# Optimization experiments

Hardware: AMD Instinct MI355X
Metric: run time of the kernel (lower is better)

## Reference

```python
import jax, jax.numpy as jnp
import numpy as np

EPS = 1e-12  # F.normalize default eps


def _l2_normalize(x):
    n = jnp.linalg.norm(x, axis=-1, keepdims=True)
    return x / jnp.maximum(n, EPS)


def setup_inputs() -> dict:
    key = jax.random.key(0)
    k1, k2 = jax.random.split(key)
    B, N, D = 2048, 100000, 256
    query = jax.random.normal(k1, (B, D), dtype=jnp.float32)
    memory_states = jax.random.normal(k2, (N, D), dtype=jnp.float32)
    return {"query": query, "memory_states": memory_states, "k": 8}


def reference(query, memory_states, k):
    # cosine-similarity retrieval: normalize both sides, dense matmul, top-k, gather
    mem_norm = _l2_normalize(memory_states)          # [N, D]
    query_norm = _l2_normalize(query)                # [B, D]
    scores = query_norm @ mem_norm.T                 # [B, N]
    top_k_scores, indices = jax.lax.top_k(scores, k)  # [B, k] each
    retrieved = memory_states[indices]               # [B, k, D] (raw, un-normalized states as in torch)
    return retrieved, top_k_scores
```

## Files before the change

### kernel.cpp

```cpp
#include <hip/hip_runtime.h>
#include <hip/hip_bf16.h>
#include <stdint.h>

#define DIM 256
#define TOPK 8
#define NSTRIPS 64
#define STRIP_TOP 8
#define QT 256
#define NT 32
#define CAND (NSTRIPS * STRIP_TOP)
#define RESCORE 64
#define IDXMASK 0x1FFFFu

typedef __attribute__((ext_vector_type(8))) short short8;
typedef __attribute__((ext_vector_type(4))) float floatx4;
typedef __attribute__((address_space(3))) unsigned int lds_u32;
typedef __attribute__((address_space(1))) const unsigned int gbl_u32;

__device__ __forceinline__ unsigned short f2bf(float f) {
    union { float f; uint32_t u; } v; v.f = f;
    uint32_t u = v.u;
    uint32_t r = u + 0x7fffu + ((u >> 16) & 1u);
    return (unsigned short)(r >> 16);
}

__device__ __forceinline__ uint32_t umaxu(uint32_t a, uint32_t b) { return a > b ? a : b; }

__device__ __forceinline__ void top8_insert(uint32_t* ts, uint32_t key) {
#pragma unroll
    for (int j = 0; j < STRIP_TOP - 1; j++) {
        uint32_t m;
        asm("v_med3_u32 %0, %1, %2, %3" : "=v"(m) : "v"(ts[j]), "v"(ts[j + 1]), "v"(key));
        ts[j] = m;
    }
    ts[STRIP_TOP - 1] = umaxu(ts[STRIP_TOP - 1], key);
}

__global__ void prep_kernel(const float* __restrict__ query,
                            const float* __restrict__ mem,
                            float* __restrict__ rnorm_mem,
                            unsigned short* __restrict__ q_bf16,
                            unsigned short* __restrict__ mem_bf16,
                            int B, int N)
{
    int wave = threadIdx.x >> 6;
    int lane = threadIdx.x & 63;
    int row  = blockIdx.x * 4 + wave;
    int total = N + B;
    if (row >= total) return;
    const float* src = (row < N) ? (mem + (size_t)row * DIM)
                                 : (query + (size_t)(row - N) * DIM);
    float4 v = ((const float4*)src)[lane];
    float ss = v.x * v.x + v.y * v.y + v.z * v.z + v.w * v.w;
#pragma unroll
    for (int m = 32; m >= 1; m >>= 1) ss += __shfl_xor(ss, m, 64);
    float rinv = 1.0f / fmaxf(sqrtf(ss), 1e-12f);
    ushort4 o;
    o.x = f2bf(v.x * rinv); o.y = f2bf(v.y * rinv);
    o.z = f2bf(v.z * rinv); o.w = f2bf(v.w * rinv);
    if (row < N) {
        if (lane == 0) rnorm_mem[row] = rinv;
        if (mem_bf16) ((ushort4*)(mem_bf16 + (size_t)row * DIM))[lane] = o;
    } else {
        ((ushort4*)(q_bf16 + (size_t)(row - N) * DIM))[lane] = o;
    }
}

template<bool PRE>
__global__ __launch_bounds__(512, 4) void score_select_kernel(
    const float* __restrict__ mem,
    const float* __restrict__ rnorm_mem,
    const unsigned short* __restrict__ mem_bf16,
    const unsigned short* __restrict__ q_bf16,
    uint32_t* __restrict__ cand_key,
    int B, int N)
{
    __shared__ unsigned short lds_m[2][NT * DIM];
    __shared__ uint32_t sc[QT * 4 * 9];

    const int t    = threadIdx.x;
    const int wave = t >> 6;
    const int lane = t & 63;
    const int quad = lane >> 4;
    const int l16  = lane & 15;

    const int lin  = (int)(blockIdx.x + gridDim.x * blockIdx.y);
    const int SPX  = NSTRIPS / 8;
    const int strip = (lin & 7) * SPX + ((lin >> 3) % SPX);
    const int qb    = (lin >> 3) / SPX;
    const int qbase = qb * QT;

    const int SS    = (N + NSTRIPS - 1) / NSTRIPS;
    const int n0    = strip * SS;
    const int nend  = (n0 + SS < N) ? (n0 + SS) : N;
    const int limit = nend - n0;
    const int ntiles = (limit + NT - 1) / NT;

    short8 qfrag[2][8];
#pragma unroll
    for (int b = 0; b < 2; b++) {
        int qrow = qbase + wave * 32 + b * 16 + l16;
        const unsigned short* qp = q_bf16 + (size_t)qrow * DIM + quad * 8;
#pragma unroll
        for (int ks = 0; ks < 8; ks++)
            qfrag[b][ks] = *(const short8*)(qp + ks * 32);
    }

    uint32_t ts[2][STRIP_TOP];
#pragma unroll
    for (int b = 0; b < 2; b++)
#pragma unroll
        for (int j = 0; j < STRIP_TOP; j++) ts[b][j] = 0;

    const int l5  = lane >> 5;
    const int s32 = lane & 31;

    auto stage = [&](unsigned short* lbase, int tileIdx) {
        int base = n0 + tileIdx * NT;
        if (PRE) {
#pragma unroll
            for (int is = 0; is < 2; is++) {
                int rl = is * 16 + wave * 2 + l5;
                int n = base + rl; if (n >= nend) n = nend - 1;
                int chunk = s32 ^ (rl & 7);
                const unsigned short* gp = mem_bf16 + (size_t)n * DIM + chunk * 8;
                unsigned short* lp = lbase + (is * 16 + wave * 2) * DIM;
                __builtin_amdgcn_global_load_lds((gbl_u32*)(const void*)gp,
                                                 (lds_u32*)(void*)lp, 16, 0, 0);
            }
        } else {
#pragma unroll
            for (int i = 0; i < 4; i++) {
                int rl = i * 8 + wave;
                int n = base + rl;
                ushort4 o;
                if (n < nend) {
                    float rinv = rnorm_mem[n];
                    float4 v = ((const float4*)(mem + (size_t)n * DIM))[lane];
                    o.x = f2bf(v.x * rinv); o.y = f2bf(v.y * rinv);
                    o.z = f2bf(v.z * rinv); o.w = f2bf(v.w * rinv);
                } else { o.x = 0; o.y = 0; o.z = 0; o.w = 0; }
                int slot = (lane >> 1) ^ (rl & 7);
                *(ushort4*)(lbase + rl * DIM + slot * 8 + (lane & 1) * 4) = o;
            }
        }
    };

    stage(&lds_m[0][0], 0);
    __syncthreads();

    const floatx4 one4 = {1.f, 1.f, 1.f, 1.f};
    for (int tile = 0; tile < ntiles; tile++) {
        unsigned short* lbuf = &lds_m[tile & 1][0];
        if (tile + 1 < ntiles) stage(&lds_m[(tile + 1) & 1][0], tile + 1);

        floatx4 acc[2][2];
#pragma unroll
        for (int a = 0; a < 2; a++)
#pragma unroll
            for (int b = 0; b < 2; b++) acc[a][b] = one4;

#pragma unroll
        for (int ks = 0; ks < 8; ks++) {
#pragma unroll
            for (int a = 0; a < 2; a++) {
                int row = a * 16 + l16;
                int slot = (ks * 4 + quad) ^ (l16 & 7);
                short8 m = *(const short8*)(lbuf + row * DIM + slot * 8);
#pragma unroll
                for (int b = 0; b < 2; b++)
                    acc[a][b] = __builtin_amdgcn_mfma_f32_16x16x32_bf16(m, qfrag[b][ks], acc[a][b], 0, 0, 0);
            }
        }

        const int tb0 = tile * NT + quad * 4;
        const bool full = (tile * NT + NT <= limit);
        if (full) {
#pragma unroll
            for (int b = 0; b < 2; b++)
#pragma unroll
                for (int a = 0; a < 2; a++)
#pragma unroll
                    for (int r = 0; r < 4; r++) {
                        uint32_t u = __float_as_uint(fmaxf(acc[a][b][r], 0.f));
                        uint32_t key = (u & 0xFFFF0000u) | (uint32_t)(tb0 + a * 16 + r);
                        top8_insert(ts[b], key);
                    }
        } else {
#pragma unroll
            for (int b = 0; b < 2; b++)
#pragma unroll
                for (int a = 0; a < 2; a++)
#pragma unroll
                    for (int r = 0; r < 4; r++) {
                        int loc = tb0 + a * 16 + r;
                        uint32_t u = __float_as_uint(fmaxf(acc[a][b][r], 0.f));
                        uint32_t key = (u & 0xFFFF0000u) | (uint32_t)loc;
                        if (loc >= limit) key = 0;
                        top8_insert(ts[b], key);
                    }
        }

        __syncthreads();
    }

#pragma unroll
    for (int b = 0; b < 2; b++)
#pragma unroll
        for (int j = 0; j < STRIP_TOP; j++)
            sc[((wave * 32 + b * 16 + l16) * 4 + quad) * 9 + j] = ts[b][j];
    __syncthreads();

    if (t < QT) {
        uint32_t best[STRIP_TOP];
#pragma unroll
        for (int j = 0; j < STRIP_TOP; j++) best[j] = sc[(t * 4 + 0) * 9 + j];
#pragma unroll
        for (int qd = 1; qd < 4; qd++)
#pragma unroll
            for (int j = 0; j < STRIP_TOP; j++)
                top8_insert(best, sc[(t * 4 + qd) * 9 + j]);

        size_t off = ((size_t)(qbase + t) * NSTRIPS + strip) * STRIP_TOP;
#pragma unroll
        for (int j = 0; j < STRIP_TOP; j++) {
            uint32_t k = best[j];
            uint32_t key2 = ((k >> 17) << 17) | (uint32_t)(n0 + (int)(k & 0xFFFFu));
            cand_key[off + j] = key2;
        }
    }
}

__global__ __launch_bounds__(256) void rescore_kernel(
    const float* __restrict__ query,
    const float* __restrict__ mem,
    const uint32_t* __restrict__ cand_key,
    float* __restrict__ out,
    int B, int N)
{
    __shared__ uint32_t cs[CAND];
    __shared__ float  lds_q[DIM];
    __shared__ double red[4];
    __shared__ double qss_sh;
    __shared__ int    sel_i[RESCORE];
    __shared__ double rs[RESCORE];
    __shared__ double best_s[TOPK];
    __shared__ int    best_i[TOPK];

    const int t    = threadIdx.x;
    const int q    = blockIdx.x;
    const int lane = t & 63;
    const int wave = t >> 6;

    for (int i = t; i < CAND; i += 256)
        cs[i] = cand_key[(size_t)q * CAND + i];

    float qv = query[(size_t)q * DIM + t];
    lds_q[t] = qv;
    double p = (double)qv * (double)qv;
#pragma unroll
    for (int m = 32; m >= 1; m >>= 1) p += __shfl_xor(p, m, 64);
    if (lane == 0) red[wave] = p;
    __syncthreads();
    if (t == 0) qss_sh = red[0] + red[1] + red[2] + red[3];

    {
        uint32_t* qcs = cs + wave * 128;
        for (int k = 2; k <= 128; k <<= 1) {
            for (int j = k >> 1; j > 0; j >>= 1) {
                int i  = 2 * lane - (lane & (j - 1));
                int ip = i + j;
                bool up = ((i & k) == 0);
                uint32_t a = qcs[i], b2 = qcs[ip];
                bool aFirst = a > b2;
                bool doSwap = up ? (!aFirst) : aFirst;
                if (doSwap) { qcs[i] = b2; qcs[ip] = a; }
            }
        }
        if (lane < 16) sel_i[wave * 16 + lane] = (int)(qcs[lane] & IDXMASK);
    }
    __syncthreads();

    double qss = qss_sh;
    for (int r = 0; r < 16; r++) {
        int c = wave * 16 + r;
        int idx = sel_i[c];
        float4 mv = ((const float4*)(mem + (size_t)idx * DIM))[lane];
        float4 qv4 = ((const float4*)lds_q)[lane];
        double dqm = (double)mv.x * (double)qv4.x + (double)mv.y * (double)qv4.y
                   + (double)mv.z * (double)qv4.z + (double)mv.w * (double)qv4.w;
        double dmm = (double)mv.x * (double)mv.x + (double)mv.y * (double)mv.y
                   + (double)mv.z * (double)mv.z + (double)mv.w * (double)mv.w;
#pragma unroll
        for (int m = 32; m >= 1; m >>= 1) {
            dqm += __shfl_xor(dqm, m, 64);
            dmm += __shfl_xor(dmm, m, 64);
        }
        if (lane == 0)
            rs[c] = dqm / (fmax(sqrt(qss), 1e-12) * fmax(sqrt(dmm), 1e-12));
    }
    __syncthreads();

    if (t == 0) {
        double bs[TOPK]; int bi[TOPK];
        for (int i = 0; i < TOPK; i++) { bs[i] = -1e300; bi[i] = 0x7fffffff; }
        for (int c = 0; c < RESCORE; c++) {
            double s = rs[c]; int id = sel_i[c];
            bool better = (s > bs[TOPK - 1]) || (s == bs[TOPK - 1] && id < bi[TOPK - 1]);
            if (better) {
                int pos = TOPK - 1;
                while (pos > 0) {
                    bool b2 = (s > bs[pos - 1]) || (s == bs[pos - 1] && id < bi[pos - 1]);
                    if (!b2) break;
                    bs[pos] = bs[pos - 1]; bi[pos] = bi[pos - 1]; pos--;
                }
                bs[pos] = s; bi[pos] = id;
            }
        }
        for (int i = 0; i < TOPK; i++) { best_s[i] = bs[i]; best_i[i] = bi[i]; }
    }
    __syncthreads();

    size_t score_base = (size_t)B * TOPK * DIM;
    if (t < TOPK) out[score_base + (size_t)q * TOPK + t] = (float)best_s[t];

#pragma unroll
    for (int rep = 0; rep < 2; rep++) {
        int j  = t >> 5;
        int d4 = (t & 31) + rep * 32;
        int idx = best_i[j];
        float4 v = ((const float4*)(mem + (size_t)idx * DIM))[d4];
        ((float4*)(out + ((size_t)q * TOPK + j) * DIM))[d4] = v;
    }
}

extern "C" void kernel_launch(void* const* d_in, const int* in_sizes, int n_in,
                              void* d_out, int out_size, void* d_ws, size_t ws_size,
                              hipStream_t stream)
{
    const float* query = (const float*)d_in[0];
    const float* mem   = (const float*)d_in[1];
    int B = in_sizes[0] / DIM;
    int N = in_sizes[1] / DIM;

    auto align256 = [](size_t x) { return (x + 255) & ~(size_t)255; };
    size_t off = 0;
    auto alloc = [&](size_t bytes) { void* p = (char*)d_ws + off; off += align256(bytes); return p; };

    float* rnorm_mem       = (float*)alloc((size_t)N * 4);
    unsigned short* q_bf16 = (unsigned short*)alloc((size_t)B * DIM * 2);
    uint32_t* cand_key     = (uint32_t*)alloc((size_t)B * CAND * 4);
    size_t base_need = off;
    unsigned short* mem_bf16 = (unsigned short*)((char*)d_ws + base_need);
    bool pre = (base_need + align256((size_t)N * DIM * 2)) <= ws_size;
    if (!pre) mem_bf16 = nullptr;

    int prep_blocks = (N + B + 3) / 4;
    prep_kernel<<<prep_blocks, 256, 0, stream>>>(query, mem, rnorm_mem, q_bf16,
                                                 mem_bf16, B, N);

    dim3 g2((B + QT - 1) / QT, NSTRIPS);
    if (pre)
        score_select_kernel<true><<<g2, 512, 0, stream>>>(mem, rnorm_mem, mem_bf16, q_bf16,
                                                          cand_key, B, N);
    else
        score_select_kernel<false><<<g2, 512, 0, stream>>>(mem, rnorm_mem, mem_bf16, q_bf16,
                                                           cand_key, B, N);

    rescore_kernel<<<B, 256, 0, stream>>>(query, mem, cand_key, (float*)d_out, B, N);
}
```

Before: 377.3 us.

## Shrink score blocks, add strips, merge per-quad top-8 via wave shuffles

Changes the scoring grid from 64 strips × 256-query blocks of 512 threads to 80 strips × 128-query blocks of 256 threads, giving more, smaller blocks for better CU balance. The final per-quad top-8 merge now uses cross-lane shuffles instead of an LDS staging buffer plus a barrier, and results are written with vector stores. The score bias is raised so the ReLU clamp can be dropped from the key construction. The rescore kernel's candidate sort grows to 1024 padded entries to fit the larger candidate count, which adds sort work per query.

```diff
diff --git a/kernel.cpp b/kernel.cpp
--- a/kernel.cpp
+++ b/kernel.cpp
@@ -4,11 +4,12 @@
 
 #define DIM 256
 #define TOPK 8
-#define NSTRIPS 64
+#define NSTRIPS 80
 #define STRIP_TOP 8
-#define QT 256
+#define QT 128
 #define NT 32
 #define CAND (NSTRIPS * STRIP_TOP)
+#define CANDPAD 1024
 #define RESCORE 64
 #define IDXMASK 0x1FFFFu
 
@@ -67,7 +68,7 @@
 }
 
 template<bool PRE>
-__global__ __launch_bounds__(512, 4) void score_select_kernel(
+__global__ __launch_bounds__(256, 4) void score_select_kernel(
     const float* __restrict__ mem,
     const float* __restrict__ rnorm_mem,
     const unsigned short* __restrict__ mem_bf16,
@@ -76,7 +77,6 @@
     int B, int N)
 {
     __shared__ unsigned short lds_m[2][NT * DIM];
-    __shared__ uint32_t sc[QT * 4 * 9];
 
     const int t    = threadIdx.x;
     const int wave = t >> 6;
@@ -119,19 +119,19 @@
         int base = n0 + tileIdx * NT;
         if (PRE) {
 #pragma unroll
-            for (int is = 0; is < 2; is++) {
-                int rl = is * 16 + wave * 2 + l5;
+            for (int is = 0; is < 4; is++) {
+                int rl = is * 8 + wave * 2 + l5;
                 int n = base + rl; if (n >= nend) n = nend - 1;
                 int chunk = s32 ^ (rl & 7);
                 const unsigned short* gp = mem_bf16 + (size_t)n * DIM + chunk * 8;
-                unsigned short* lp = lbase + (is * 16 + wave * 2) * DIM;
+                unsigned short* lp = lbase + (is * 8 + wave * 2) * DIM;
                 __builtin_amdgcn_global_load_lds((gbl_u32*)(const void*)gp,
                                                  (lds_u32*)(void*)lp, 16, 0, 0);
             }
         } else {
 #pragma unroll
-            for (int i = 0; i < 4; i++) {
-                int rl = i * 8 + wave;
+            for (int i = 0; i < 8; i++) {
+                int rl = i * 4 + wave;
                 int n = base + rl;
                 ushort4 o;
                 if (n < nend) {
@@ -149,7 +149,7 @@
     stage(&lds_m[0][0], 0);
     __syncthreads();
 
-    const floatx4 one4 = {1.f, 1.f, 1.f, 1.f};
+    const floatx4 bias4 = {1.125f, 1.125f, 1.125f, 1.125f};
     for (int tile = 0; tile < ntiles; tile++) {
         unsigned short* lbuf = &lds_m[tile & 1][0];
         if (tile + 1 < ntiles) stage(&lds_m[(tile + 1) & 1][0], tile + 1);
@@ -158,7 +158,7 @@
 #pragma unroll
         for (int a = 0; a < 2; a++)
 #pragma unroll
-            for (int b = 0; b < 2; b++) acc[a][b] = one4;
+            for (int b = 0; b < 2; b++) acc[a][b] = bias4;
 
 #pragma unroll
         for (int ks = 0; ks < 8; ks++) {
@@ -182,7 +182,7 @@
                 for (int a = 0; a < 2; a++)
 #pragma unroll
                     for (int r = 0; r < 4; r++) {
-                        uint32_t u = __float_as_uint(fmaxf(acc[a][b][r], 0.f));
+                        uint32_t u = __float_as_uint(acc[a][b][r]);
                         uint32_t key = (u & 0xFFFF0000u) | (uint32_t)(tb0 + a * 16 + r);
                         top8_insert(ts[b], key);
                     }
@@ -194,7 +194,7 @@
 #pragma unroll
                     for (int r = 0; r < 4; r++) {
                         int loc = tb0 + a * 16 + r;
-                        uint32_t u = __float_as_uint(fmaxf(acc[a][b][r], 0.f));
+                        uint32_t u = __float_as_uint(acc[a][b][r]);
                         uint32_t key = (u & 0xFFFF0000u) | (uint32_t)loc;
                         if (loc >= limit) key = 0;
                         top8_insert(ts[b], key);
@@ -205,28 +205,36 @@
     }
 
 #pragma unroll
-    for (int b = 0; b < 2; b++)
-#pragma unroll
-        for (int j = 0; j < STRIP_TOP; j++)
-            sc[((wave * 32 + b * 16 + l16) * 4 + quad) * 9 + j] = ts[b][j];
-    __syncthreads();
-
-    if (t < QT) {
-        uint32_t best[STRIP_TOP];
-#pragma unroll
-        for (int j = 0; j < STRIP_TOP; j++) best[j] = sc[(t * 4 + 0) * 9 + j];
-#pragma unroll
-        for (int qd = 1; qd < 4; qd++)
+    for (int b = 0; b < 2; b++) {
+#pragma unroll
+        for (int step = 32; step >= 16; step >>= 1) {
+            uint32_t other[STRIP_TOP];
 #pragma unroll
             for (int j = 0; j < STRIP_TOP; j++)
-                top8_insert(best, sc[(t * 4 + qd) * 9 + j]);
-
-        size_t off = ((size_t)(qbase + t) * NSTRIPS + strip) * STRIP_TOP;
-#pragma unroll
-        for (int j = 0; j < STRIP_TOP; j++) {
-            uint32_t k = best[j];
-            uint32_t key2 = ((k >> 17) << 17) | (uint32_t)(n0 + (int)(k & 0xFFFFu));
-            cand_key[off + j] = key2;
+                other[j] = __shfl_xor(ts[b][j], step, 64);
+#pragma unroll
+            for (int j = 0; j < STRIP_TOP; j++)
+                top8_insert(ts[b], other[j]);
+        }
+    }
+
+    if (quad == 0) {
+#pragma unroll
+        for (int b = 0; b < 2; b++) {
+            int q = qbase + wave * 32 + b * 16 + l16;
+            size_t off = ((size_t)q * NSTRIPS + strip) * STRIP_TOP;
+            uint4 o0, o1;
+            uint32_t k;
+            k = ts[b][0]; o0.x = ((k >> 17) << 17) | (uint32_t)(n0 + (int)(k & 0xFFFFu));
+            k = ts[b][1]; o0.y = ((k >> 17) << 17) | (uint32_t)(n0 + (int)(k & 0xFFFFu));
+            k = ts[b][2]; o0.z = ((k >> 17) << 17) | (uint32_t)(n0 + (int)(k & 0xFFFFu));
+            k = ts[b][3]; o0.w = ((k >> 17) << 17) | (uint32_t)(n0 + (int)(k & 0xFFFFu));
+            k = ts[b][4]; o1.x = ((k >> 17) << 17) | (uint32_t)(n0 + (int)(k & 0xFFFFu));
+            k = ts[b][5]; o1.y = ((k >> 17) << 17) | (uint32_t)(n0 + (int)(k & 0xFFFFu));
+            k = ts[b][6]; o1.z = ((k >> 17) << 17) | (uint32_t)(n0 + (int)(k & 0xFFFFu));
+            k = ts[b][7]; o1.w = ((k >> 17) << 17) | (uint32_t)(n0 + (int)(k & 0xFFFFu));
+            ((uint4*)(cand_key + off))[0] = o0;
+            ((uint4*)(cand_key + off))[1] = o1;
         }
     }
 }
@@ -238,7 +246,7 @@
     float* __restrict__ out,
     int B, int N)
 {
-    __shared__ uint32_t cs[CAND];
+    __shared__ uint32_t cs[CANDPAD];
     __shared__ float  lds_q[DIM];
     __shared__ double red[4];
     __shared__ double qss_sh;
@@ -252,8 +260,8 @@
     const int lane = t & 63;
     const int wave = t >> 6;
 
-    for (int i = t; i < CAND; i += 256)
-        cs[i] = cand_key[(size_t)q * CAND + i];
+    for (int i = t; i < CANDPAD; i += 256)
+        cs[i] = (i < CAND) ? cand_key[(size_t)q * CAND + i] : 0u;
 
     float qv = query[(size_t)q * DIM + t];
     lds_q[t] = qv;
@@ -265,16 +273,20 @@
     if (t == 0) qss_sh = red[0] + red[1] + red[2] + red[3];
 
     {
-        uint32_t* qcs = cs + wave * 128;
-        for (int k = 2; k <= 128; k <<= 1) {
+        uint32_t* qcs = cs + wave * 256;
+        for (int k = 2; k <= 256; k <<= 1) {
             for (int j = k >> 1; j > 0; j >>= 1) {
-                int i  = 2 * lane - (lane & (j - 1));
-                int ip = i + j;
-                bool up = ((i & k) == 0);
-                uint32_t a = qcs[i], b2 = qcs[ip];
-                bool aFirst = a > b2;
-                bool doSwap = up ? (!aFirst) : aFirst;
-                if (doSwap) { qcs[i] = b2; qcs[ip] = a; }
+#pragma unroll
+                for (int rep = 0; rep < 2; rep++) {
+                    int c  = lane + rep * 64;
+                    int i  = 2 * c - (c & (j - 1));
+                    int ip = i + j;
+                    bool up = ((i & k) == 0);
+                    uint32_t a = qcs[i], b2 = qcs[ip];
+                    bool aFirst = a > b2;
+                    bool doSwap = up ? (!aFirst) : aFirst;
+                    if (doSwap) { qcs[i] = b2; qcs[ip] = a; }
+                }
             }
         }
         if (lane < 16) sel_i[wave * 16 + lane] = (int)(qcs[lane] & IDXMASK);
@@ -361,10 +373,10 @@
 
     dim3 g2((B + QT - 1) / QT, NSTRIPS);
     if (pre)
-        score_select_kernel<true><<<g2, 512, 0, stream>>>(mem, rnorm_mem, mem_bf16, q_bf16,
+        score_select_kernel<true><<<g2, 256, 0, stream>>>(mem, rnorm_mem, mem_bf16, q_bf16,
                                                           cand_key, B, N);
     else
-        score_select_kernel<false><<<g2, 512, 0, stream>>>(mem, rnorm_mem, mem_bf16, q_bf16,
+        score_select_kernel<false><<<g2, 256, 0, stream>>>(mem, rnorm_mem, mem_bf16, q_bf16,
                                                            cand_key, B, N);
 
     rescore_kernel<<<B, 256, 0, stream>>>(query, mem, cand_key, (float*)d_out, B, N);
```

New measurement: 482.1 us. 27.8% more time.
